# Kernel optimization log

Measured on AMD Instinct MI355X. Metric: run time of the kernel, lower is better.

Reference implementation:

```python
import jax, jax.numpy as jnp
from jax import lax
import numpy as np

B, T, C_IN, H, W = 2, 4, 128, 64, 64
D_MODEL, N_Q, N_POINTS, PATCH, N_LAYERS = 256, 300, 8, 3, 6


def _sine_pos(Hh, Ww, d, temperature=10000.0):
    # mask is all-False, so cumsum of ones -> arange(1..H)/H * 2pi
    two_pi = 2.0 * np.pi
    yn = (jnp.arange(1, Hh + 1, dtype=jnp.float32) / (Hh + 1e-6)) * two_pi
    xn = (jnp.arange(1, Ww + 1, dtype=jnp.float32) / (Ww + 1e-6)) * two_pi
    q = d // 4
    i = jnp.arange(q, dtype=jnp.float32)
    dim_t = temperature ** (2.0 * jnp.floor(i / 2.0) / q)
    py = yn[:, None] / dim_t
    px = xn[:, None] / dim_t
    py = jnp.stack([jnp.sin(py), jnp.cos(py)], axis=-1).reshape(Hh, 2 * q)
    px = jnp.stack([jnp.sin(px), jnp.cos(px)], axis=-1).reshape(Ww, 2 * q)
    pos = jnp.concatenate([
        jnp.broadcast_to(py[:, None, :], (Hh, Ww, 2 * q)),
        jnp.broadcast_to(px[None, :, :], (Hh, Ww, 2 * q)),
    ], axis=-1)
    return jnp.transpose(pos, (2, 0, 1))  # [d,H,W]


def _sample_scale(fmap, ref, ps):
    # fmap [B,C,h,w]; ref [B,nQ,nP,2] in [0,1]. Bilinear grid_sample,
    # padding_mode='border', align_corners=True -> direct gather (no replication).
    Bc, C, h, w = fmap.shape
    half = (ps - 1) / 2.0
    off = jnp.linspace(-half, half, ps, dtype=jnp.float32)
    oy, ox = jnp.meshgrid(off, off, indexing='ij')  # [ps,ps]
    gx = ref[..., 0, None, None] * 2.0 - 1.0 + ox * (2.0 / w)  # [B,nQ,nP,ps,ps]
    gy = ref[..., 1, None, None] * 2.0 - 1.0 + oy * (2.0 / h)
    x = jnp.clip((gx + 1.0) * 0.5 * (w - 1), 0.0, w - 1.0)
    y = jnp.clip((gy + 1.0) * 0.5 * (h - 1), 0.0, h - 1.0)
    x0 = jnp.floor(x); y0 = jnp.floor(y)
    wx = x - x0; wy = y - y0
    x0i = x0.astype(jnp.int32); y0i = y0.astype(jnp.int32)
    x1i = jnp.minimum(x0i + 1, w - 1); y1i = jnp.minimum(y0i + 1, h - 1)

    def per_b(fb, y0b, x0b, y1b, x1b, wxb, wyb):
        v00 = fb[:, y0b, x0b]  # [C,nQ,nP,ps,ps]
        v01 = fb[:, y0b, x1b]
        v10 = fb[:, y1b, x0b]
        v11 = fb[:, y1b, x1b]
        return (v00 * (1 - wxb) * (1 - wyb) + v01 * wxb * (1 - wyb)
                + v10 * (1 - wxb) * wyb + v11 * wxb * wyb)

    out = jax.vmap(per_b)(fmap, y0i, x0i, y1i, x1i, wx, wy)  # [B,C,nQ,nP,ps,ps]
    return jnp.transpose(out, (0, 2, 3, 4, 5, 1))  # [B,nQ,nP,ps,ps,C]


def reference(feat, pred_boxes_init, w_tf, b_tf, w_in, b_in, w_lat, b_lat, w_sm, b_sm,
              q_embed, q_pos, Wq, bq, Wo, bo, Wp1, bp1, Wp2, bp2,
              w_r1, b_r1, w_r2, b_r2, w_b1, b_b1, w_b2, b_b2, w_cls, b_cls):
    Bb, Tt, Cin, Hh, Ww = feat.shape
    d = w_in.shape[0]
    nP = w_r2.shape[0] // 2
    ps = int(round((Wp1.shape[-1] // d) ** 0.5))
    # temporal fuse: Conv3d kernel (3,1,1), padding (1,0,0)
    x = lax.conv_general_dilated(jnp.transpose(feat, (0, 2, 1, 3, 4)), w_tf,
                                 (1, 1, 1), [(1, 1), (0, 0), (0, 0)],
                                 dimension_numbers=('NCDHW', 'OIDHW', 'NCDHW'))
    x = x + b_tf[None, :, None, None, None]
    x = x.mean(axis=2)  # [B,Cin,H,W]
    x = jnp.einsum('bchw,dc->bdhw', x, w_in) + b_in[None, :, None, None]
    x = x + _sine_pos(Hh, Ww, d)[None]
    # FPN over scales {1,2,4}: avg_pool -> 1x1 lateral -> 3x3 smooth
    feats = []
    for i, s in enumerate((1, 2, 4)):
        xi = x if s == 1 else x.reshape(Bb, d, Hh // s, s, Ww // s, s).mean(axis=(3, 5))
        xi = jnp.einsum('bchw,oc->bohw', xi, w_lat[i]) + b_lat[i][None, :, None, None]
        xi = lax.conv_general_dilated(xi, w_sm[i], (1, 1), [(1, 1), (1, 1)],
                                      dimension_numbers=('NCHW', 'OIHW', 'NCHW'))
        xi = xi + b_sm[i][None, :, None, None]
        feats.append(xi)
    nQ = q_embed.shape[0]
    queries = jnp.broadcast_to((q_embed + q_pos)[None], (Bb, nQ, d))
    boxes = pred_boxes_init
    inv_sqrt_d = 1.0 / float(np.sqrt(d))
    for l in range(Wq.shape[0]):
        h1 = jax.nn.relu(jnp.einsum('bqd,od->bqo', queries, w_r1) + b_r1)
        ro = jnp.tanh(jnp.einsum('bqd,od->bqo', h1, w_r2) + b_r2)
        ro = ro.reshape(Bb, nQ, nP, 2) * 0.5
        ref = jnp.clip(boxes[:, :, None, :2] + ro, 0.0, 1.0)
        sampled = jnp.concatenate([_sample_scale(f, ref, ps) for f in feats], axis=2)
        sampled = sampled[:, :, :nP]  # truncate multi-scale concat back to nP
        flat = sampled.reshape(Bb, nQ, nP, ps * ps * d)
        pv = jax.nn.relu(jnp.einsum('bqpi,oi->bqpo', flat, Wp1[l]) + bp1[l])
        pv = jnp.einsum('bqpd,od->bqpo', pv, Wp2[l]) + bp2[l]
        kv = pv.mean(axis=2)  # [B,nP_q,d] -> [B,nQ,d]
        q = jnp.einsum('bqd,od->bqo', queries, Wq[l]) + bq[l]
        attn = jax.nn.softmax(jnp.einsum('bqd,bkd->bqk', q, kv) * inv_sqrt_d, axis=-1)
        out = jnp.einsum('bqk,bkd->bqd', attn, kv)
        queries = queries + (jnp.einsum('bqd,od->bqo', out, Wo[l]) + bo[l])
        hb = jax.nn.relu(jnp.einsum('bqd,od->bqo', queries, w_b1) + b_b1)
        delta = jax.nn.sigmoid(jnp.einsum('bqd,od->bqo', hb, w_b2) + b_b2)
        boxes = jnp.clip(boxes + 0.1 * jnp.tanh(delta - 0.5), 0.0, 1.0)
    logits = (jnp.einsum('bqd,od->bqo', queries, w_cls) + b_cls)[..., 0]
    return logits, boxes


def setup_inputs() -> dict:
    key = jax.random.key(0)
    keys = iter(jax.random.split(key, 48))

    def nrm(shape, s=0.02):
        return jax.random.normal(next(keys), shape, dtype=jnp.float32) * s

    inp = {
        'feat': jax.random.normal(next(keys), (B, T, C_IN, H, W), dtype=jnp.float32),
        'pred_boxes_init': jax.random.uniform(next(keys), (B, N_Q, 4), dtype=jnp.float32),
        'w_tf': nrm((C_IN, C_IN, 3, 1, 1)), 'b_tf': jnp.zeros((C_IN,), jnp.float32),
        'w_in': nrm((D_MODEL, C_IN)), 'b_in': jnp.zeros((D_MODEL,), jnp.float32),
        'w_lat': nrm((3, D_MODEL, D_MODEL)), 'b_lat': jnp.zeros((3, D_MODEL), jnp.float32),
        'w_sm': nrm((3, D_MODEL, D_MODEL, 3, 3)), 'b_sm': jnp.zeros((3, D_MODEL), jnp.float32),
        'q_embed': nrm((N_Q, D_MODEL), 1.0), 'q_pos': nrm((N_Q, D_MODEL), 1.0),
        'Wq': nrm((N_LAYERS, D_MODEL, D_MODEL)), 'bq': jnp.zeros((N_LAYERS, D_MODEL), jnp.float32),
        'Wo': nrm((N_LAYERS, D_MODEL, D_MODEL)), 'bo': jnp.zeros((N_LAYERS, D_MODEL), jnp.float32),
        'Wp1': nrm((N_LAYERS, D_MODEL, PATCH * PATCH * D_MODEL)), 'bp1': jnp.zeros((N_LAYERS, D_MODEL), jnp.float32),
        'Wp2': nrm((N_LAYERS, D_MODEL, D_MODEL)), 'bp2': jnp.zeros((N_LAYERS, D_MODEL), jnp.float32),
        'w_r1': nrm((D_MODEL, D_MODEL)), 'b_r1': jnp.zeros((D_MODEL,), jnp.float32),
        'w_r2': nrm((2 * N_POINTS, D_MODEL)), 'b_r2': jnp.zeros((2 * N_POINTS,), jnp.float32),
        'w_b1': nrm((D_MODEL, D_MODEL)), 'b_b1': jnp.zeros((D_MODEL,), jnp.float32),
        'w_b2': nrm((4, D_MODEL)), 'b_b2': jnp.zeros((4,), jnp.float32),
        'w_cls': nrm((1, D_MODEL)), 'b_cls': jnp.zeros((1,), jnp.float32),
    }
    return inp
```

## Files before the change

### kernel.cpp

```cpp
#include <hip/hip_runtime.h>
#include <hip/hip_bf16.h>
#include <math.h>

#define BB 2
#define TT 4
#define CIN 128
#define DM 256
#define NQ 300
#define NP 8
#define PS 3
#define NL 6
#define HW 4096
#define KP 2304

typedef __attribute__((ext_vector_type(8))) short short8;
typedef __attribute__((ext_vector_type(4))) short short4_t;
typedef __attribute__((ext_vector_type(4))) float f32x4;
typedef unsigned short ushort_t;

static __device__ __forceinline__ ushort_t f2bf(float f) {
  __hip_bfloat16 h = __float2bfloat16(f);
  return *reinterpret_cast<ushort_t*>(&h);
}
static __device__ __forceinline__ float bf2f(ushort_t u) {
  return __uint_as_float(((unsigned)u) << 16);
}

__global__ void k_prep(const float* __restrict__ w_in, const float* __restrict__ w_lat,
                       const float* __restrict__ Wp2, const float* __restrict__ Wo,
                       const float* __restrict__ w_b1, const float* __restrict__ Wp1,
                       ushort_t* __restrict__ win_bf, ushort_t* __restrict__ wlat_bf,
                       ushort_t* __restrict__ wp2_bf, ushort_t* __restrict__ wo_bf,
                       ushort_t* __restrict__ wb1_bf, ushort_t* __restrict__ wp1_bf,
                       const float* __restrict__ w_tf, ushort_t* __restrict__ tct,
                       const float* __restrict__ w_sm, ushort_t* __restrict__ wsm_bf,
                       const float* __restrict__ w_r1, const float* __restrict__ Wq,
                       ushort_t* __restrict__ wqr_bf,
                       const float* __restrict__ b_r1, const float* __restrict__ bq,
                       float* __restrict__ bqr,
                       uint4* __restrict__ x2p_zero,
                       const float* __restrict__ b_tf, const float* __restrict__ b_in,
                       float* __restrict__ bias_comb,
                       const float* __restrict__ qe, const float* __restrict__ qp,
                       const float* __restrict__ pb, float* __restrict__ queries,
                       ushort_t* __restrict__ qbf, float* __restrict__ boxes) {
  __shared__ float bt[128];
  int b = blockIdx.x, t = threadIdx.x;
  if (b < 4385) {
    int i = b * 256 + t;
    const float* s; ushort_t* d; int base;
    if (i < 8192)         { s = w_in;  d = win_bf;  base = 0; }
    else if (i < 24576)   { s = w_lat; d = wlat_bf; base = 8192; }
    else if (i < 122880)  { s = Wp2;   d = wp2_bf;  base = 24576; }
    else if (i < 221184)  { s = Wo;    d = wo_bf;   base = 122880; }
    else if (i < 237568)  { s = w_b1;  d = wb1_bf;  base = 221184; }
    else if (i < 1122304) { s = Wp1;   d = wp1_bf;  base = 237568; }
    else return;
    int j = i - base;
    float4 v = ((const float4*)s)[j];
    d[j * 4 + 0] = f2bf(v.x);
    d[j * 4 + 1] = f2bf(v.y);
    d[j * 4 + 2] = f2bf(v.z);
    d[j * 4 + 3] = f2bf(v.w);
  } else if (b < 4641) {
    int i = (b - 4385) * 256 + t;
    int k = i >> 7, c = i & 127;
    int u = k >> 7, ci = k & 127;
    const float* wp = w_tf + ((size_t)(c * 128 + ci)) * 3;
    float w0 = wp[0], w1 = wp[1], w2 = wp[2];
    float coef = (u == 0) ? (w0 + w1) : (u == 3) ? (w1 + w2) : (w0 + w1 + w2);
    tct[(size_t)k * 128 + c] = f2bf(0.25f * coef);
  } else if (b < 6945) {
    int i = (b - 4641) * 256 + t;
    int n = i / KP;
    int r = i - n * KP;
    int tp = r >> 8, c = r & 255;
    wsm_bf[i] = f2bf(w_sm[((size_t)(n * 256 + c)) * 9 + tp]);
  } else if (b < 10017) {
    int i = (b - 6945) * 256 + t;
    int l = i / (512 * 256);
    int r = i - l * 512 * 256;
    int n = r >> 8, c = r & 255;
    float v = (n < 256) ? w_r1[n * 256 + c] : Wq[((size_t)l * 256 + (n - 256)) * 256 + c];
    wqr_bf[i] = f2bf(v);
  } else if (b < 10029) {
    int i = (b - 10017) * 256 + t;
    if (i >= NL * 512) return;
    int l = i >> 9, n = i & 511;
    bqr[i] = (n < 256) ? b_r1[n] : bq[l * 256 + n - 256];
  } else if (b < 11118) {
    int j = (b - 10029) * 256 + t;
    if (j < 278784) x2p_zero[j] = make_uint4(0u, 0u, 0u, 0u);
  } else if (b < 11119) {
    int d = t;
    if (d < 128) bt[d] = b_tf[d];
    __syncthreads();
    float a = b_in[d];
    for (int c = 0; c < 128; ++c) a += w_in[d * 128 + c] * bt[c];
    bias_comb[d] = a;
  } else {
    int i = (b - 11119) * 256 + t;
    if (i < BB * NQ * DM) {
      int rd = i % (NQ * DM);
      float v = qe[rd] + qp[rd];
      queries[i] = v;
      qbf[i] = f2bf(v);
    }
    if (i < BB * NQ * 4) boxes[i] = pb[i];
  }
}

__global__ __launch_bounds__(256) void k_tr(const float* __restrict__ feat,
                                            ushort_t* __restrict__ featT) {
  __shared__ float ldsF[64][65];
  int tid = threadIdx.x;
  int gs = blockIdx.x;
  int b = gs >> 6;
  int s0 = (gs & 63) * 64;
  int k0 = blockIdx.y * 64;
  int kk = tid >> 2, sc0 = (tid & 3) * 16;
  {
    int k = k0 + kk;
    int u = k >> 7, ci = k & 127;
    const float* src = feat + (((size_t)(b * 4 + u) * 128 + ci) << 12) + s0 + sc0;
#pragma unroll
    for (int j = 0; j < 4; ++j) {
      float4 v = *(const float4*)(src + j * 4);
      ldsF[kk][sc0 + j * 4 + 0] = v.x;
      ldsF[kk][sc0 + j * 4 + 1] = v.y;
      ldsF[kk][sc0 + j * 4 + 2] = v.z;
      ldsF[kk][sc0 + j * 4 + 3] = v.w;
    }
  }
  __syncthreads();
#pragma unroll
  for (int p = 0; p < 2; ++p) {
    int idx = p * 256 + tid;
    int s_l = idx >> 3, kc = (idx & 7) * 8;
    short8 v;
#pragma unroll
    for (int j = 0; j < 8; ++j) v[j] = (short)f2bf(ldsF[kc + j][s_l]);
    *(short8*)(featT + (size_t)(b * 4096 + s0 + s_l) * 512 + k0 + kc) = v;
  }
}

__global__ __launch_bounds__(256) void k_feat2(const ushort_t* __restrict__ featT,
                                               const ushort_t* __restrict__ wcomb,
                                               const float* __restrict__ biasc,
                                               ushort_t* __restrict__ xcl) {
  __shared__ ushort_t As[32 * 36];
  __shared__ ushort_t Bs[64 * 36];
  __shared__ float dimt_s[256];
  int tid = threadIdx.x;
  {
    int dd = tid & 127;
    int ii = dd >> 1;
    dimt_s[tid] = powf(10000.0f, (2.0f * (float)(ii >> 1)) / 64.0f);
  }
  int bm = blockIdx.x * 32, bn = blockIdx.y * 64;
  int w = tid >> 6, lane = tid & 63;
  int wm = (w & 1) * 16, wn = (w >> 1) * 32;
  int q = lane >> 4, ml = lane & 15;
  int sra = tid >> 3, sca = (tid & 7) * 4;
  int srb = tid >> 2, scb = (tid & 3) * 8;
  const ushort_t* Ag = featT + (size_t)(bm + sra) * 512 + sca;
  const ushort_t* Wg = wcomb + (size_t)(bn + srb) * 512 + scb;
  f32x4 acc[2] = {};
  short4_t av = *(const short4_t*)Ag;
  short8 wv = *(const short8*)Wg;
  for (int k0 = 0; k0 < 512; k0 += 32) {
    *(short4_t*)(As + sra * 36 + sca) = av;
    *(short8*)(Bs + srb * 36 + scb) = wv;
    __syncthreads();
    if (k0 + 32 < 512) {
      av = *(const short4_t*)(Ag + k0 + 32);
      wv = *(const short8*)(Wg + k0 + 32);
    }
    short8 a = *(const short8*)(As + (wm + ml) * 36 + q * 8);
    short8 b0 = *(const short8*)(Bs + (wn + ml) * 36 + q * 8);
    short8 b1 = *(const short8*)(Bs + (wn + 16 + ml) * 36 + q * 8);
    acc[0] = __builtin_amdgcn_mfma_f32_16x16x32_bf16(a, b0, acc[0], 0, 0, 0);
    acc[1] = __builtin_amdgcn_mfma_f32_16x16x32_bf16(a, b1, acc[1], 0, 0, 0);
    __syncthreads();
  }
  const float FKT = 6.28318530717958647692f / 64.000001f;
#pragma unroll
  for (int j = 0; j < 2; ++j) {
    int cn = bn + wn + j * 16 + ml;
    float dimt = dimt_s[cn];
    float bC = biasc[cn];
    bool isx = cn >= 128;
    bool isc = cn & 1;
#pragma unroll
    for (int r = 0; r < 4; ++r) {
      int rm = bm + wm + q * 4 + r;
      int s = rm & 4095;
      int y = s >> 6, x = s & 63;
      float ang = (float)((isx ? x : y) + 1) * FKT / dimt;
      float pos = isc ? cosf(ang) : sinf(ang);
      xcl[(size_t)rm * 256 + cn] = f2bf(acc[j][r] + bC + pos);
    }
  }
}

template <int ACT, int OUTMODE, int MG>
__global__ __launch_bounds__(256) void k_gemm_bf16(const ushort_t* __restrict__ A,
                                                   const ushort_t* __restrict__ W,
                                                   const float* __restrict__ bias,
                                                   const float* __restrict__ res,
                                                   float* __restrict__ Cf,
                                                   ushort_t* __restrict__ Cb,
                                                   int M, int N, int K,
                                                   const ushort_t* __restrict__ W2,
                                                   const float* __restrict__ bias2) {
  __shared__ ushort_t As[64 * 36];
  __shared__ ushort_t Bs[64 * 36];
  int tid = threadIdx.x;
  int bm = blockIdx.x * 64, bn = blockIdx.y * 64;
  int w = tid >> 6, lane = tid & 63;
  int wm = (w & 1) * 32, wn = (w >> 1) * 32;
  int q = lane >> 4, ml = lane & 15;
  f32x4 acc[2][2] = {};
  int srow = tid >> 2, scol = (tid & 3) * 8;
  int ga = bm + srow;
  if (MG) ga = min(ga, M - 1);
  const ushort_t* Ag = A + (size_t)ga * K + scol;
  const ushort_t* Wg;
  if (OUTMODE == 7 && bn >= 256) Wg = W2 + (size_t)(bn - 256 + srow) * K + scol;
  else Wg = W + (size_t)(bn + srow) * K + scol;
  for (int k0 = 0; k0 < K; k0 += 32) {
    short8 av = *(const short8*)(Ag + k0);
    short8 wv = *(const short8*)(Wg + k0);
    *(short8*)(As + srow * 36 + scol) = av;
    *(short8*)(Bs + srow * 36 + scol) = wv;
    __syncthreads();
    short8 a0 = *(const short8*)(As + (wm + ml) * 36 + q * 8);
    short8 a1 = *(const short8*)(As + (wm + 16 + ml) * 36 + q * 8);
    short8 b0 = *(const short8*)(Bs + (wn + ml) * 36 + q * 8);
    short8 b1 = *(const short8*)(Bs + (wn + 16 + ml) * 36 + q * 8);
    acc[0][0] = __builtin_amdgcn_mfma_f32_16x16x32_bf16(a0, b0, acc[0][0], 0, 0, 0);
    acc[0][1] = __builtin_amdgcn_mfma_f32_16x16x32_bf16(a0, b1, acc[0][1], 0, 0, 0);
    acc[1][0] = __builtin_amdgcn_mfma_f32_16x16x32_bf16(a1, b0, acc[1][0], 0, 0, 0);
    acc[1][1] = __builtin_amdgcn_mfma_f32_16x16x32_bf16(a1, b1, acc[1][1], 0, 0, 0);
    __syncthreads();
  }
#pragma unroll
  for (int i = 0; i < 2; ++i) {
#pragma unroll
    for (int j = 0; j < 2; ++j) {
      int cn = bn + wn + j * 16 + ml;
      float bsv;
      if (OUTMODE == 7) bsv = (cn < 256) ? bias[cn] : bias2[cn - 256];
      else bsv = bias ? bias[cn] : 0.f;
#pragma unroll
      for (int r = 0; r < 4; ++r) {
        int rm = bm + wm + i * 16 + q * 4 + r;
        if (MG && rm >= M) continue;
        float v = acc[i][j][r] + bsv;
        if (OUTMODE == 0) {
          if (ACT == 1) v = fmaxf(v, 0.f);
          Cf[(size_t)rm * N + cn] = v;
        } else if (OUTMODE == 1) {
          int b = rm >> 12, rem = rm & 4095;
          int y = rem >> 6, xx = rem & 63;
          Cb[(((size_t)(b * 66 + y + 1)) * 66 + xx + 1) * 256 + cn] = f2bf(v);
        } else if (OUTMODE == 2) {
          v += res[(size_t)rm * N + cn];
          Cf[(size_t)rm * N + cn] = v;
          Cb[(size_t)rm * N + cn] = f2bf(v);
        } else if (OUTMODE == 4) {
          if (cn < 256) Cf[(size_t)rm * 256 + cn] = fmaxf(v, 0.f);
          else Cb[(size_t)rm * 256 + cn - 256] = f2bf(v);
        } else if (OUTMODE == 6) {
          Cb[(size_t)rm * N + cn] = f2bf(v);
        } else if (OUTMODE == 7) {
          if (cn < 256) Cf[(size_t)rm * 256 + cn] = fmaxf(v, 0.f);
          else if (cn < 512) ((float*)Cb)[(size_t)rm * 256 + cn - 256] = fmaxf(v, 0.f);
          else ((ushort_t*)res)[(size_t)rm * 256 + cn - 512] = f2bf(v);
        }
      }
    }
  }
}

__global__ __launch_bounds__(256) void k_wp1_split(const ushort_t* __restrict__ A,
                                                   const ushort_t* __restrict__ W,
                                                   float* __restrict__ part) {
  __shared__ ushort_t As[64 * 36];
  __shared__ ushort_t Bs[64 * 36];
  int tid = threadIdx.x;
  int bm = blockIdx.x * 64, bn = blockIdx.y * 64;
  int kz = blockIdx.z * 768;
  int w = tid >> 6, lane = tid & 63;
  int wm = (w & 1) * 32, wn = (w >> 1) * 32;
  int q = lane >> 4, ml = lane & 15;
  int srow = tid >> 2, scol = (tid & 3) * 8;
  const ushort_t* Ag = A + (size_t)(bm + srow) * KP + kz + scol;
  const ushort_t* Wg = W + (size_t)(bn + srow) * KP + kz + scol;
  f32x4 acc[2][2] = {};
  short8 av = *(const short8*)(Ag);
  short8 wv = *(const short8*)(Wg);
  for (int k0 = 0; k0 < 768; k0 += 32) {
    *(short8*)(As + srow * 36 + scol) = av;
    *(short8*)(Bs + srow * 36 + scol) = wv;
    __syncthreads();
    if (k0 + 32 < 768) {
      av = *(const short8*)(Ag + k0 + 32);
      wv = *(const short8*)(Wg + k0 + 32);
    }
    short8 a0 = *(const short8*)(As + (wm + ml) * 36 + q * 8);
    short8 a1 = *(const short8*)(As + (wm + 16 + ml) * 36 + q * 8);
    short8 b0 = *(const short8*)(Bs + (wn + ml) * 36 + q * 8);
    short8 b1 = *(const short8*)(Bs + (wn + 16 + ml) * 36 + q * 8);
    acc[0][0] = __builtin_amdgcn_mfma_f32_16x16x32_bf16(a0, b0, acc[0][0], 0, 0, 0);
    acc[0][1] = __builtin_amdgcn_mfma_f32_16x16x32_bf16(a0, b1, acc[0][1], 0, 0, 0);
    acc[1][0] = __builtin_amdgcn_mfma_f32_16x16x32_bf16(a1, b0, acc[1][0], 0, 0, 0);
    acc[1][1] = __builtin_amdgcn_mfma_f32_16x16x32_bf16(a1, b1, acc[1][1], 0, 0, 0);
    __syncthreads();
  }
  float* pz = part + (size_t)blockIdx.z * 4800 * 256;
#pragma unroll
  for (int i = 0; i < 2; ++i)
#pragma unroll
    for (int j = 0; j < 2; ++j) {
      int cn = bn + wn + j * 16 + ml;
#pragma unroll
      for (int r = 0; r < 4; ++r) {
        int rm = bm + wm + i * 16 + q * 4 + r;
        pz[(size_t)rm * 256 + cn] = acc[i][j][r];
      }
    }
}

__global__ __launch_bounds__(256) void k_wp1_reduce(const float* __restrict__ part,
                                                    const float* __restrict__ bias,
                                                    ushort_t* __restrict__ pvm) {
  int row = blockIdx.x;
  int d = threadIdx.x;
  float b = bias[d];
  float s = 0.f;
#pragma unroll
  for (int p = 0; p < 8; ++p) {
    size_t idx = (size_t)(row * 8 + p) * 256 + d;
    float v = part[idx] + part[idx + (size_t)4800 * 256] +
              part[idx + (size_t)2 * 4800 * 256] + b;
    s += fmaxf(v, 0.f);
  }
  pvm[(size_t)row * 256 + d] = f2bf(s * 0.125f);
}

__global__ __launch_bounds__(256) void k_conv3(const ushort_t* __restrict__ x2p,
                                               const ushort_t* __restrict__ wsm,
                                               const float* __restrict__ bsm,
                                               ushort_t* __restrict__ fcl) {
  __shared__ ushort_t As[32 * 36];
  __shared__ ushort_t Bs[64 * 36];
  int tid = threadIdx.x;
  int bm = blockIdx.x * 32, bn = blockIdx.y * 64;
  int w = tid >> 6, lane = tid & 63;
  int wm = (w & 1) * 16, wn = (w >> 1) * 32;
  int q = lane >> 4, ml = lane & 15;
  int sra = tid >> 3, sca = (tid & 7) * 4;
  int srb = tid >> 2, scb = (tid & 3) * 8;
  int sA = bm + sra;
  int b = sA >> 12, rem = sA & 4095;
  size_t pbase = ((size_t)(b * 66 + (rem >> 6)) * 66 + (rem & 63)) * 256;
  const ushort_t* Wg = wsm + (size_t)(bn + srb) * KP + scb;
  auto loadA = [&](int k0) {
    int ka = k0 + sca;
    int t9 = ka >> 8;
    int ky = t9 / 3, kx = t9 - ky * 3;
    return *(const short4_t*)(x2p + pbase + (size_t)(ky * 66 + kx) * 256 + (ka & 255));
  };
  f32x4 acc[2] = {};
  short4_t av = loadA(0);
  short8 wv = *(const short8*)(Wg);
  for (int k0 = 0; k0 < KP; k0 += 32) {
    *(short4_t*)(As + sra * 36 + sca) = av;
    *(short8*)(Bs + srb * 36 + scb) = wv;
    __syncthreads();
    if (k0 + 32 < KP) {
      av = loadA(k0 + 32);
      wv = *(const short8*)(Wg + k0 + 32);
    }
    short8 a = *(const short8*)(As + (wm + ml) * 36 + q * 8);
    short8 b0 = *(const short8*)(Bs + (wn + ml) * 36 + q * 8);
    short8 b1 = *(const short8*)(Bs + (wn + 16 + ml) * 36 + q * 8);
    acc[0] = __builtin_amdgcn_mfma_f32_16x16x32_bf16(a, b0, acc[0], 0, 0, 0);
    acc[1] = __builtin_amdgcn_mfma_f32_16x16x32_bf16(a, b1, acc[1], 0, 0, 0);
    __syncthreads();
  }
#pragma unroll
  for (int j = 0; j < 2; ++j) {
    int cn = bn + wn + j * 16 + ml;
    float bsv = bsm[cn];
#pragma unroll
    for (int r = 0; r < 4; ++r) {
      int rm = bm + wm + q * 4 + r;
      fcl[(size_t)rm * 256 + cn] = f2bf(acc[j][r] + bsv);
    }
  }
}

__global__ __launch_bounds__(256) void k_sample(const ushort_t* __restrict__ fcl,
                                                const float* __restrict__ h1,
                                                const float* __restrict__ w_r2,
                                                const float* __restrict__ b_r2,
                                                const float* __restrict__ boxes,
                                                ushort_t* __restrict__ flat) {
  __shared__ float pr[8];
  __shared__ float bc2[2];
  int blk = blockIdx.x;
  int row = blk >> 3, p = blk & 7;
  int b = row / NQ;
  int tid = threadIdx.x;
  float h = h1[(size_t)row * 256 + tid];
  float px = h * w_r2[(size_t)(2 * p) * 256 + tid];
  float py = h * w_r2[(size_t)(2 * p + 1) * 256 + tid];
#pragma unroll
  for (int s = 32; s > 0; s >>= 1) {
    px += __shfl_down(px, s, 64);
    py += __shfl_down(py, s, 64);
  }
  int w = tid >> 6, lane = tid & 63;
  if (lane == 0) { pr[w * 2] = px; pr[w * 2 + 1] = py; }
  __syncthreads();
  if (tid == 0) {
    float sx = pr[0] + pr[2] + pr[4] + pr[6] + b_r2[2 * p];
    float sy = pr[1] + pr[3] + pr[5] + pr[7] + b_r2[2 * p + 1];
    float rx = boxes[row * 4 + 0] + 0.5f * tanhf(sx);
    float ry = boxes[row * 4 + 1] + 0.5f * tanhf(sy);
    bc2[0] = fminf(fmaxf(rx, 0.f), 1.f);
    bc2[1] = fminf(fmaxf(ry, 0.f), 1.f);
  }
  __syncthreads();
  float rx = bc2[0], ry = bc2[1];
  int c = tid;
  const ushort_t* fb = fcl + (size_t)b * HW * DM;
  ushort_t* op = flat + (size_t)blk * KP;
#pragma unroll
  for (int jy = 0; jy < 3; ++jy) {
    float yy = (ry + (float)(jy - 1) * (1.0f / 64.0f)) * 63.0f;
    yy = fminf(fmaxf(yy, 0.f), 63.0f);
    float y0f = floorf(yy);
    float wy = yy - y0f;
    int y0 = (int)y0f;
    int y1 = min(y0 + 1, 63);
#pragma unroll
    for (int jx = 0; jx < 3; ++jx) {
      float xx = (rx + (float)(jx - 1) * (1.0f / 64.0f)) * 63.0f;
      xx = fminf(fmaxf(xx, 0.f), 63.0f);
      float x0f = floorf(xx);
      float wx = xx - x0f;
      int x0 = (int)x0f;
      int x1 = min(x0 + 1, 63);
      float v00 = bf2f(fb[(y0 * 64 + x0) * DM + c]);
      float v01 = bf2f(fb[(y0 * 64 + x1) * DM + c]);
      float v10 = bf2f(fb[(y1 * 64 + x0) * DM + c]);
      float v11 = bf2f(fb[(y1 * 64 + x1) * DM + c]);
      float v = v00 * (1.f - wx) * (1.f - wy) + v01 * wx * (1.f - wy) +
                v10 * (1.f - wx) * wy + v11 * wx * wy;
      op[(jy * 3 + jx) * DM + c] = f2bf(v);
    }
  }
}

__global__ __launch_bounds__(256) void k_attn(const ushort_t* __restrict__ qb2,
                                              const ushort_t* __restrict__ kvb,
                                              ushort_t* __restrict__ ao) {
  __shared__ float qs[256];
  __shared__ float sc[512];
  __shared__ float red[256];
  int row = blockIdx.x;
  int b = row / NQ;
  int tid = threadIdx.x;
  qs[tid] = bf2f(qb2[(size_t)row * DM + tid]);
  __syncthreads();
  const ushort_t* kvB = kvb + (size_t)b * NQ * DM;
#pragma unroll
  for (int s2 = 0; s2 < 2; ++s2) {
    int k = tid + s2 * 256;
    float v = -1e30f;
    if (k < NQ) {
      const ushort_t* kp = kvB + (size_t)k * DM;
      float a = 0.f;
#pragma unroll
      for (int d = 0; d < 256; d += 8) {
        short8 k8 = *(const short8*)(kp + d);
        const float* qd = qs + d;
        a += bf2f((ushort_t)k8[0]) * qd[0];
        a += bf2f((ushort_t)k8[1]) * qd[1];
        a += bf2f((ushort_t)k8[2]) * qd[2];
        a += bf2f((ushort_t)k8[3]) * qd[3];
        a += bf2f((ushort_t)k8[4]) * qd[4];
        a += bf2f((ushort_t)k8[5]) * qd[5];
        a += bf2f((ushort_t)k8[6]) * qd[6];
        a += bf2f((ushort_t)k8[7]) * qd[7];
      }
      v = a * (1.0f / 16.0f);
    }
    sc[k] = v;
  }
  __syncthreads();
  red[tid] = fmaxf(sc[tid], sc[tid + 256]);
  __syncthreads();
  for (int st = 128; st > 0; st >>= 1) {
    if (tid < st) red[tid] = fmaxf(red[tid], red[tid + st]);
    __syncthreads();
  }
  float mx = red[0];
  __syncthreads();
  float e0 = (tid < NQ) ? expf(sc[tid] - mx) : 0.f;
  float e1 = (tid + 256 < NQ) ? expf(sc[tid + 256] - mx) : 0.f;
  sc[tid] = e0;
  sc[tid + 256] = e1;
  red[tid] = e0 + e1;
  __syncthreads();
  for (int st = 128; st > 0; st >>= 1) {
    if (tid < st) red[tid] += red[tid + st];
    __syncthreads();
  }
  float inv = 1.0f / red[0];
  __syncthreads();
  float acc = 0.f;
#pragma unroll 4
  for (int k = 0; k < NQ; ++k)
    acc += sc[k] * bf2f(kvB[(size_t)k * DM + tid]);
  ao[(size_t)row * DM + tid] = f2bf(acc * inv);
}

__global__ __launch_bounds__(256) void k_boxf(const float* __restrict__ hb,
                                              const float* __restrict__ w_b2,
                                              const float* __restrict__ b_b2,
                                              float* __restrict__ boxes,
                                              int last,
                                              const float* __restrict__ queries,
                                              const float* __restrict__ w_cls,
                                              const float* __restrict__ b_cls,
                                              float* __restrict__ out) {
  __shared__ float nb[4];
  int row = blockIdx.x;
  int tid = threadIdx.x;
  int j = tid >> 6, lane = tid & 63;
  float4 hv = *(const float4*)(hb + (size_t)row * 256 + lane * 4);
  float4 wv = *(const float4*)(w_b2 + (size_t)j * 256 + lane * 4);
  float aa = hv.x * wv.x + hv.y * wv.y + hv.z * wv.z + hv.w * wv.w;
#pragma unroll
  for (int s = 32; s > 0; s >>= 1) aa += __shfl_down(aa, s, 64);
  if (lane == 0) {
    aa += b_b2[j];
    float delta = 1.0f / (1.0f + expf(-aa));
    float v = boxes[row * 4 + j] + 0.1f * tanhf(delta - 0.5f);
    v = fminf(fmaxf(v, 0.f), 1.f);
    boxes[row * 4 + j] = v;
    nb[j] = v;
  }
  if (last) {
    __syncthreads();
    if (j == 0) {
      float4 qv = *(const float4*)(queries + (size_t)row * 256 + lane * 4);
      float4 cv = *(const float4*)(w_cls + lane * 4);
      float a2 = qv.x * cv.x + qv.y * cv.y + qv.z * cv.z + qv.w * cv.w;
#pragma unroll
      for (int s = 32; s > 0; s >>= 1) a2 += __shfl_down(a2, s, 64);
      if (lane == 0) out[row] = a2 + b_cls[0];
    } else if (j == 1 && lane < 4) {
      out[600 + row * 4 + lane] = nb[lane];
    }
  }
}

extern "C" void kernel_launch(void* const* d_in, const int* in_sizes, int n_in,
                              void* d_out, int out_size, void* d_ws, size_t ws_size,
                              hipStream_t stream) {
  const float* feat   = (const float*)d_in[0];
  const float* pb     = (const float*)d_in[1];
  const float* w_tf   = (const float*)d_in[2];
  const float* b_tf   = (const float*)d_in[3];
  const float* w_in   = (const float*)d_in[4];
  const float* b_in   = (const float*)d_in[5];
  const float* w_lat  = (const float*)d_in[6];
  const float* b_lat  = (const float*)d_in[7];
  const float* w_sm   = (const float*)d_in[8];
  const float* b_sm   = (const float*)d_in[9];
  const float* q_embed= (const float*)d_in[10];
  const float* q_pos  = (const float*)d_in[11];
  const float* Wq     = (const float*)d_in[12];
  const float* bq     = (const float*)d_in[13];
  const float* Wo     = (const float*)d_in[14];
  const float* bo     = (const float*)d_in[15];
  const float* Wp1    = (const float*)d_in[16];
  const float* bp1    = (const float*)d_in[17];
  const float* Wp2    = (const float*)d_in[18];
  const float* bp2    = (const float*)d_in[19];
  const float* w_r1   = (const float*)d_in[20];
  const float* b_r1   = (const float*)d_in[21];
  const float* w_r2   = (const float*)d_in[22];
  const float* b_r2   = (const float*)d_in[23];
  const float* w_b1   = (const float*)d_in[24];
  const float* b_b1   = (const float*)d_in[25];
  const float* w_b2   = (const float*)d_in[26];
  const float* b_b2   = (const float*)d_in[27];
  const float* w_cls  = (const float*)d_in[28];
  const float* b_cls  = (const float*)d_in[29];
  float* out = (float*)d_out;

  float* ws = (float*)d_ws;
  size_t off = 0;
  auto alloc = [&](size_t n) { float* p = ws + off; off += n; return p; };
  ushort_t* flat    = (ushort_t*)alloc(5529600);
  float*    part    = alloc(3686400);
  ushort_t* featT   = (ushort_t*)alloc(2097152);
  ushort_t* xcl     = (ushort_t*)alloc(1048576);
  ushort_t* x2p     = (ushort_t*)alloc(1115136);
  ushort_t* fcl     = (ushort_t*)alloc(1048576);
  ushort_t* wcomb   = (ushort_t*)alloc(65536);
  ushort_t* tct     = (ushort_t*)alloc(32768);
  ushort_t* win_bf  = (ushort_t*)alloc(16384);
  float*    biasc   = alloc(256);
  ushort_t* wlat_bf = (ushort_t*)alloc(32768);
  ushort_t* wsm_bf  = (ushort_t*)alloc(294912);
  ushort_t* wp1_bf  = (ushort_t*)alloc(1769472);
  ushort_t* wqr_bf  = (ushort_t*)alloc(393216);
  float*    bqr     = alloc(3072);
  ushort_t* wp2_bf  = (ushort_t*)alloc(196608);
  ushort_t* wo_bf   = (ushort_t*)alloc(196608);
  ushort_t* wb1_bf  = (ushort_t*)alloc(32768);
  float* queries = alloc(153600);
  ushort_t* qbf  = (ushort_t*)alloc(76800);
  float* h1      = alloc(153600);
  ushort_t* qb2  = (ushort_t*)alloc(76800);
  ushort_t* kvb  = (ushort_t*)alloc(76800);
  ushort_t* ao   = (ushort_t*)alloc(76800);
  float* hb      = alloc(153600);
  ushort_t* pvm  = (ushort_t*)alloc(76800);
  float* boxes   = alloc(2400);
  (void)ws_size; (void)in_sizes; (void)n_in; (void)out_size;

  k_prep<<<11719, 256, 0, stream>>>(w_in, w_lat, Wp2, Wo, w_b1, Wp1,
                                    win_bf, wlat_bf, wp2_bf, wo_bf, wb1_bf, wp1_bf,
                                    w_tf, tct, w_sm, wsm_bf, w_r1, Wq, wqr_bf,
                                    b_r1, bq, bqr,
                                    (uint4*)x2p, b_tf, b_in, biasc,
                                    q_embed, q_pos, pb, queries, qbf, boxes);
  k_gemm_bf16<0, 6, 0><<<dim3(4, 8), 256, 0, stream>>>(win_bf, tct, nullptr, nullptr,
                                                       nullptr, wcomb, 256, 512, 128,
                                                       nullptr, nullptr);
  k_tr<<<dim3(128, 8), 256, 0, stream>>>(feat, featT);
  k_feat2<<<dim3(256, 4), 256, 0, stream>>>(featT, wcomb, biasc, xcl);
  k_gemm_bf16<0, 1, 0><<<dim3(128, 4), 256, 0, stream>>>(xcl, wlat_bf, b_lat, nullptr,
                                                         nullptr, x2p, BB * HW, 256, 256,
                                                         nullptr, nullptr);
  k_conv3<<<dim3(256, 4), 256, 0, stream>>>(x2p, wsm_bf, b_sm, fcl);

  const int M6 = BB * NQ;
  const int Mp = BB * NQ * NP;
  dim3 g600((M6 + 63) / 64, 4);
  dim3 g600w((M6 + 63) / 64, 8);
  dim3 g600m((M6 + 63) / 64, 12);
  dim3 gsk(Mp / 64, 4, 3);

  k_gemm_bf16<0, 4, 1><<<g600w, 256, 0, stream>>>(qbf, wqr_bf, bqr, nullptr, h1,
                                                  qb2, M6, 512, 256,
                                                  nullptr, nullptr);
  for (int l = 0; l < NL; ++l) {
    k_sample<<<Mp, 256, 0, stream>>>(fcl, h1, w_r2, b_r2, boxes, flat);
    k_wp1_split<<<gsk, 256, 0, stream>>>(flat, wp1_bf + (size_t)l * 256 * KP, part);
    k_wp1_reduce<<<600, 256, 0, stream>>>(part, bp1 + (size_t)l * DM, pvm);
    k_gemm_bf16<0, 6, 1><<<g600, 256, 0, stream>>>(pvm, wp2_bf + (size_t)l * DM * DM,
                                                   bp2 + (size_t)l * DM, nullptr, nullptr,
                                                   kvb, M6, DM, DM, nullptr, nullptr);
    k_attn<<<M6, 256, 0, stream>>>(qb2, kvb, ao);
    k_gemm_bf16<0, 2, 1><<<g600, 256, 0, stream>>>(ao, wo_bf + (size_t)l * DM * DM,
                                                   bo + (size_t)l * DM, queries, queries,
                                                   qbf, M6, DM, DM, nullptr, nullptr);
    int ln = (l + 1) % NL;
    k_gemm_bf16<0, 7, 1><<<g600m, 256, 0, stream>>>(qbf, wb1_bf, b_b1, (const float*)qb2,
                                                    hb, (ushort_t*)h1, M6, 768, 256,
                                                    wqr_bf + (size_t)ln * 512 * 256,
                                                    bqr + ln * 512);
    k_boxf<<<M6, 256, 0, stream>>>(hb, w_b2, b_b2, boxes, (l == NL - 1) ? 1 : 0,
                                   queries, w_cls, b_cls, out);
  }
}
```

Measured before the change: 775.2 us.

## Fold Wp2 into query and output projections, store split-K partials in bf16

Removes the per-layer Wp2 GEMM by algebraically composing it into the attention path. The query projection is pre-multiplied by Wp2, so scores use pvm directly. Wo is composed with Wp2 into a fused output weight, with matching fused biases computed in a new compose kernel at setup. Split-K partials for Wp1 are also stored as bf16 to halve that traffic, at the cost of extra rounding from bf16-composed weights and partials.

```diff
diff --git a/kernel.cpp b/kernel.cpp
--- a/kernel.cpp
+++ b/kernel.cpp
@@ -27,17 +27,18 @@
 }
 
 __global__ void k_prep(const float* __restrict__ w_in, const float* __restrict__ w_lat,
-                       const float* __restrict__ Wp2, const float* __restrict__ Wo,
-                       const float* __restrict__ w_b1, const float* __restrict__ Wp1,
+                       const float* __restrict__ Wo, const float* __restrict__ w_b1,
+                       const float* __restrict__ w_r1, const float* __restrict__ Wp1,
                        ushort_t* __restrict__ win_bf, ushort_t* __restrict__ wlat_bf,
-                       ushort_t* __restrict__ wp2_bf, ushort_t* __restrict__ wo_bf,
-                       ushort_t* __restrict__ wb1_bf, ushort_t* __restrict__ wp1_bf,
+                       ushort_t* __restrict__ wo_bf, ushort_t* __restrict__ wb1_bf,
+                       ushort_t* __restrict__ wr1_bf, ushort_t* __restrict__ wp1_bf,
                        const float* __restrict__ w_tf, ushort_t* __restrict__ tct,
                        const float* __restrict__ w_sm, ushort_t* __restrict__ wsm_bf,
-                       const float* __restrict__ w_r1, const float* __restrict__ Wq,
-                       ushort_t* __restrict__ wqr_bf,
-                       const float* __restrict__ b_r1, const float* __restrict__ bq,
-                       float* __restrict__ bqr,
+                       const float* __restrict__ Wp2, const float* __restrict__ Wq,
+                       ushort_t* __restrict__ wp2t, ushort_t* __restrict__ wqT,
+                       const float* __restrict__ bq, const float* __restrict__ bp2,
+                       const float* __restrict__ bo,
+                       float* __restrict__ bqt, float* __restrict__ bfuse,
                        uint4* __restrict__ x2p_zero,
                        const float* __restrict__ b_tf, const float* __restrict__ b_in,
                        float* __restrict__ bias_comb,
@@ -46,52 +47,67 @@
                        ushort_t* __restrict__ qbf, float* __restrict__ boxes) {
   __shared__ float bt[128];
   int b = blockIdx.x, t = threadIdx.x;
-  if (b < 4385) {
+  if (b < 4064) {
     int i = b * 256 + t;
     const float* s; ushort_t* d; int base;
     if (i < 8192)         { s = w_in;  d = win_bf;  base = 0; }
     else if (i < 24576)   { s = w_lat; d = wlat_bf; base = 8192; }
-    else if (i < 122880)  { s = Wp2;   d = wp2_bf;  base = 24576; }
-    else if (i < 221184)  { s = Wo;    d = wo_bf;   base = 122880; }
-    else if (i < 237568)  { s = w_b1;  d = wb1_bf;  base = 221184; }
-    else if (i < 1122304) { s = Wp1;   d = wp1_bf;  base = 237568; }
-    else return;
+    else if (i < 122880)  { s = Wo;    d = wo_bf;   base = 24576; }
+    else if (i < 139264)  { s = w_b1;  d = wb1_bf;  base = 122880; }
+    else if (i < 155648)  { s = w_r1;  d = wr1_bf;  base = 139264; }
+    else                  { s = Wp1;   d = wp1_bf;  base = 155648; }
     int j = i - base;
     float4 v = ((const float4*)s)[j];
     d[j * 4 + 0] = f2bf(v.x);
     d[j * 4 + 1] = f2bf(v.y);
     d[j * 4 + 2] = f2bf(v.z);
     d[j * 4 + 3] = f2bf(v.w);
-  } else if (b < 4641) {
-    int i = (b - 4385) * 256 + t;
+  } else if (b < 4320) {
+    int i = (b - 4064) * 256 + t;
     int k = i >> 7, c = i & 127;
     int u = k >> 7, ci = k & 127;
     const float* wp = w_tf + ((size_t)(c * 128 + ci)) * 3;
     float w0 = wp[0], w1 = wp[1], w2 = wp[2];
     float coef = (u == 0) ? (w0 + w1) : (u == 3) ? (w1 + w2) : (w0 + w1 + w2);
     tct[(size_t)k * 128 + c] = f2bf(0.25f * coef);
-  } else if (b < 6945) {
-    int i = (b - 4641) * 256 + t;
+  } else if (b < 6624) {
+    int i = (b - 4320) * 256 + t;
     int n = i / KP;
     int r = i - n * KP;
     int tp = r >> 8, c = r & 255;
     wsm_bf[i] = f2bf(w_sm[((size_t)(n * 256 + c)) * 9 + tp]);
-  } else if (b < 10017) {
-    int i = (b - 6945) * 256 + t;
-    int l = i / (512 * 256);
-    int r = i - l * 512 * 256;
-    int n = r >> 8, c = r & 255;
-    float v = (n < 256) ? w_r1[n * 256 + c] : Wq[((size_t)l * 256 + (n - 256)) * 256 + c];
-    wqr_bf[i] = f2bf(v);
-  } else if (b < 10029) {
-    int i = (b - 10017) * 256 + t;
-    if (i >= NL * 512) return;
-    int l = i >> 9, n = i & 511;
-    bqr[i] = (n < 256) ? b_r1[n] : bq[l * 256 + n - 256];
-  } else if (b < 11118) {
-    int j = (b - 10029) * 256 + t;
+  } else if (b < 9696) {
+    int i = (b - 6624) * 256 + t;
+    if (i < 393216) {
+      int l = i >> 16, r = i & 65535;
+      int d = r >> 8, o = r & 255;
+      wp2t[i] = f2bf(Wp2[((size_t)(l * 256 + o)) * 256 + d]);
+    } else {
+      int j = i - 393216;
+      int l = j >> 16, r = j & 65535;
+      int c = r >> 8, o = r & 255;
+      wqT[j] = f2bf(Wq[((size_t)(l * 256 + o)) * 256 + c]);
+    }
+  } else if (b < 9708) {
+    int i = (b - 9696) * 256 + t;
+    if (i < 1536) {
+      int l = i >> 8, d = i & 255;
+      float a = 0.f;
+      for (int o = 0; o < 256; ++o)
+        a += bq[l * 256 + o] * Wp2[((size_t)(l * 256 + o)) * 256 + d];
+      bqt[i] = a;
+    } else {
+      int j = i - 1536;
+      int l = j >> 8, o2 = j & 255;
+      float a = bo[l * 256 + o2];
+      for (int o = 0; o < 256; ++o)
+        a += bp2[l * 256 + o] * Wo[((size_t)(l * 256 + o2)) * 256 + o];
+      bfuse[j] = a;
+    }
+  } else if (b < 10797) {
+    int j = (b - 9708) * 256 + t;
     if (j < 278784) x2p_zero[j] = make_uint4(0u, 0u, 0u, 0u);
-  } else if (b < 11119) {
+  } else if (b < 10798) {
     int d = t;
     if (d < 128) bt[d] = b_tf[d];
     __syncthreads();
@@ -99,7 +115,7 @@
     for (int c = 0; c < 128; ++c) a += w_in[d * 128 + c] * bt[c];
     bias_comb[d] = a;
   } else {
-    int i = (b - 11119) * 256 + t;
+    int i = (b - 10798) * 256 + t;
     if (i < BB * NQ * DM) {
       int rd = i % (NQ * DM);
       float v = qe[rd] + qp[rd];
@@ -108,6 +124,57 @@
     }
     if (i < BB * NQ * 4) boxes[i] = pb[i];
   }
+}
+
+__global__ __launch_bounds__(256) void k_wcompose(const ushort_t* __restrict__ wp2t,
+                                                  const ushort_t* __restrict__ wqT,
+                                                  const ushort_t* __restrict__ wo_bf,
+                                                  ushort_t* __restrict__ wqt,
+                                                  ushort_t* __restrict__ wfuse) {
+  __shared__ ushort_t As[64 * 36];
+  __shared__ ushort_t Bs[64 * 36];
+  int z = blockIdx.z, l = z % 6;
+  const ushort_t* A;
+  const ushort_t* W;
+  ushort_t* C;
+  if (z < 6) { A = wp2t + l * 65536; W = wqT + l * 65536; C = wqt + l * 65536; }
+  else       { A = wo_bf + l * 65536; W = wp2t + l * 65536; C = wfuse + l * 65536; }
+  int tid = threadIdx.x;
+  int bm = blockIdx.x * 64, bn = blockIdx.y * 64;
+  int w = tid >> 6, lane = tid & 63;
+  int wm = (w & 1) * 32, wn = (w >> 1) * 32;
+  int q = lane >> 4, ml = lane & 15;
+  f32x4 acc[2][2] = {};
+  int srow = tid >> 2, scol = (tid & 3) * 8;
+  const ushort_t* Ag = A + (size_t)(bm + srow) * 256 + scol;
+  const ushort_t* Wg = W + (size_t)(bn + srow) * 256 + scol;
+  for (int k0 = 0; k0 < 256; k0 += 32) {
+    short8 av = *(const short8*)(Ag + k0);
+    short8 wv = *(const short8*)(Wg + k0);
+    *(short8*)(As + srow * 36 + scol) = av;
+    *(short8*)(Bs + srow * 36 + scol) = wv;
+    __syncthreads();
+    short8 a0 = *(const short8*)(As + (wm + ml) * 36 + q * 8);
+    short8 a1 = *(const short8*)(As + (wm + 16 + ml) * 36 + q * 8);
+    short8 b0 = *(const short8*)(Bs + (wn + ml) * 36 + q * 8);
+    short8 b1 = *(const short8*)(Bs + (wn + 16 + ml) * 36 + q * 8);
+    acc[0][0] = __builtin_amdgcn_mfma_f32_16x16x32_bf16(a0, b0, acc[0][0], 0, 0, 0);
+    acc[0][1] = __builtin_amdgcn_mfma_f32_16x16x32_bf16(a0, b1, acc[0][1], 0, 0, 0);
+    acc[1][0] = __builtin_amdgcn_mfma_f32_16x16x32_bf16(a1, b0, acc[1][0], 0, 0, 0);
+    acc[1][1] = __builtin_amdgcn_mfma_f32_16x16x32_bf16(a1, b1, acc[1][1], 0, 0, 0);
+    __syncthreads();
+  }
+#pragma unroll
+  for (int i = 0; i < 2; ++i)
+#pragma unroll
+    for (int j = 0; j < 2; ++j) {
+      int cn = bn + wn + j * 16 + ml;
+#pragma unroll
+      for (int r = 0; r < 4; ++r) {
+        int rm = bm + wm + i * 16 + q * 4 + r;
+        C[(size_t)rm * 256 + cn] = f2bf(acc[i][j][r]);
+      }
+    }
 }
 
 __global__ __launch_bounds__(256) void k_tr(const float* __restrict__ feat,
@@ -212,7 +279,9 @@
                                                    ushort_t* __restrict__ Cb,
                                                    int M, int N, int K,
                                                    const ushort_t* __restrict__ W2,
-                                                   const float* __restrict__ bias2) {
+                                                   const float* __restrict__ bias2,
+                                                   const ushort_t* __restrict__ W3,
+                                                   const float* __restrict__ bias3) {
   __shared__ ushort_t As[64 * 36];
   __shared__ ushort_t Bs[64 * 36];
   int tid = threadIdx.x;
@@ -226,8 +295,16 @@
   if (MG) ga = min(ga, M - 1);
   const ushort_t* Ag = A + (size_t)ga * K + scol;
   const ushort_t* Wg;
-  if (OUTMODE == 7 && bn >= 256) Wg = W2 + (size_t)(bn - 256 + srow) * K + scol;
-  else Wg = W + (size_t)(bn + srow) * K + scol;
+  if (OUTMODE == 7) {
+    int seg = bn >> 8;
+    const ushort_t* Wb = (seg == 0) ? W : ((seg == 1) ? W2 : W3);
+    Wg = Wb + (size_t)((bn & 255) + srow) * K + scol;
+  } else if (OUTMODE == 4) {
+    const ushort_t* Wb = (bn < 256) ? W : W2;
+    Wg = Wb + (size_t)((bn & 255) + srow) * K + scol;
+  } else {
+    Wg = W + (size_t)(bn + srow) * K + scol;
+  }
   for (int k0 = 0; k0 < K; k0 += 32) {
     short8 av = *(const short8*)(Ag + k0);
     short8 wv = *(const short8*)(Wg + k0);
@@ -250,8 +327,14 @@
     for (int j = 0; j < 2; ++j) {
       int cn = bn + wn + j * 16 + ml;
       float bsv;
-      if (OUTMODE == 7) bsv = (cn < 256) ? bias[cn] : bias2[cn - 256];
-      else bsv = bias ? bias[cn] : 0.f;
+      if (OUTMODE == 7) {
+        int seg = cn >> 8;
+        bsv = ((seg == 0) ? bias : ((seg == 1) ? bias2 : bias3))[cn & 255];
+      } else if (OUTMODE == 4) {
+        bsv = ((cn < 256) ? bias : bias2)[cn & 255];
+      } else {
+        bsv = bias ? bias[cn] : 0.f;
+      }
 #pragma unroll
       for (int r = 0; r < 4; ++r) {
         int rm = bm + wm + i * 16 + q * 4 + r;
@@ -270,13 +353,13 @@
           Cb[(size_t)rm * N + cn] = f2bf(v);
         } else if (OUTMODE == 4) {
           if (cn < 256) Cf[(size_t)rm * 256 + cn] = fmaxf(v, 0.f);
-          else Cb[(size_t)rm * 256 + cn - 256] = f2bf(v);
+          else Cb[(size_t)rm * 256 + (cn & 255)] = f2bf(v);
         } else if (OUTMODE == 6) {
           Cb[(size_t)rm * N + cn] = f2bf(v);
         } else if (OUTMODE == 7) {
           if (cn < 256) Cf[(size_t)rm * 256 + cn] = fmaxf(v, 0.f);
-          else if (cn < 512) ((float*)Cb)[(size_t)rm * 256 + cn - 256] = fmaxf(v, 0.f);
-          else ((ushort_t*)res)[(size_t)rm * 256 + cn - 512] = f2bf(v);
+          else if (cn < 512) ((float*)Cb)[(size_t)rm * 256 + (cn & 255)] = fmaxf(v, 0.f);
+          else ((ushort_t*)res)[(size_t)rm * 256 + (cn & 255)] = f2bf(v);
         }
       }
     }
@@ -285,7 +368,7 @@
 
 __global__ __launch_bounds__(256) void k_wp1_split(const ushort_t* __restrict__ A,
                                                    const ushort_t* __restrict__ W,
-                                                   float* __restrict__ part) {
+                                                   ushort_t* __restrict__ part) {
   __shared__ ushort_t As[64 * 36];
   __shared__ ushort_t Bs[64 * 36];
   int tid = threadIdx.x;
@@ -318,7 +401,7 @@
     acc[1][1] = __builtin_amdgcn_mfma_f32_16x16x32_bf16(a1, b1, acc[1][1], 0, 0, 0);
     __syncthreads();
   }
-  float* pz = part + (size_t)blockIdx.z * 4800 * 256;
+  ushort_t* pz = part + (size_t)blockIdx.z * 4800 * 256;
 #pragma unroll
   for (int i = 0; i < 2; ++i)
 #pragma unroll
@@ -327,12 +410,12 @@
 #pragma unroll
       for (int r = 0; r < 4; ++r) {
         int rm = bm + wm + i * 16 + q * 4 + r;
-        pz[(size_t)rm * 256 + cn] = acc[i][j][r];
+        pz[(size_t)rm * 256 + cn] = f2bf(acc[i][j][r]);
       }
     }
 }
 
-__global__ __launch_bounds__(256) void k_wp1_reduce(const float* __restrict__ part,
+__global__ __launch_bounds__(256) void k_wp1_reduce(const ushort_t* __restrict__ part,
                                                     const float* __restrict__ bias,
                                                     ushort_t* __restrict__ pvm) {
   int row = blockIdx.x;
@@ -342,8 +425,8 @@
 #pragma unroll
   for (int p = 0; p < 8; ++p) {
     size_t idx = (size_t)(row * 8 + p) * 256 + d;
-    float v = part[idx] + part[idx + (size_t)4800 * 256] +
-              part[idx + (size_t)2 * 4800 * 256] + b;
+    float v = bf2f(part[idx]) + bf2f(part[idx + (size_t)4800 * 256]) +
+              bf2f(part[idx + (size_t)2 * 4800 * 256]) + b;
     s += fmaxf(v, 0.f);
   }
   pvm[(size_t)row * 256 + d] = f2bf(s * 0.125f);
@@ -465,18 +548,18 @@
   }
 }
 
-__global__ __launch_bounds__(256) void k_attn(const ushort_t* __restrict__ qb2,
-                                              const ushort_t* __restrict__ kvb,
-                                              ushort_t* __restrict__ ao) {
+__global__ __launch_bounds__(256) void k_attn(const ushort_t* __restrict__ qt,
+                                              const ushort_t* __restrict__ pvm,
+                                              ushort_t* __restrict__ ctx) {
   __shared__ float qs[256];
   __shared__ float sc[512];
   __shared__ float red[256];
   int row = blockIdx.x;
   int b = row / NQ;
   int tid = threadIdx.x;
-  qs[tid] = bf2f(qb2[(size_t)row * DM + tid]);
-  __syncthreads();
-  const ushort_t* kvB = kvb + (size_t)b * NQ * DM;
+  qs[tid] = bf2f(qt[(size_t)row * DM + tid]);
+  __syncthreads();
+  const ushort_t* kvB = pvm + (size_t)b * NQ * DM;
 #pragma unroll
   for (int s2 = 0; s2 < 2; ++s2) {
     int k = tid + s2 * 256;
@@ -526,7 +609,7 @@
 #pragma unroll 4
   for (int k = 0; k < NQ; ++k)
     acc += sc[k] * bf2f(kvB[(size_t)k * DM + tid]);
-  ao[(size_t)row * DM + tid] = f2bf(acc * inv);
+  ctx[(size_t)row * DM + tid] = f2bf(acc * inv);
 }
 
 __global__ __launch_bounds__(256) void k_boxf(const float* __restrict__ hb,
@@ -609,7 +692,7 @@
   size_t off = 0;
   auto alloc = [&](size_t n) { float* p = ws + off; off += n; return p; };
   ushort_t* flat    = (ushort_t*)alloc(5529600);
-  float*    part    = alloc(3686400);
+  ushort_t* part    = (ushort_t*)alloc(1843200);
   ushort_t* featT   = (ushort_t*)alloc(2097152);
   ushort_t* xcl     = (ushort_t*)alloc(1048576);
   ushort_t* x2p     = (ushort_t*)alloc(1115136);
@@ -621,36 +704,42 @@
   ushort_t* wlat_bf = (ushort_t*)alloc(32768);
   ushort_t* wsm_bf  = (ushort_t*)alloc(294912);
   ushort_t* wp1_bf  = (ushort_t*)alloc(1769472);
-  ushort_t* wqr_bf  = (ushort_t*)alloc(393216);
-  float*    bqr     = alloc(3072);
-  ushort_t* wp2_bf  = (ushort_t*)alloc(196608);
   ushort_t* wo_bf   = (ushort_t*)alloc(196608);
   ushort_t* wb1_bf  = (ushort_t*)alloc(32768);
+  ushort_t* wr1_bf  = (ushort_t*)alloc(32768);
+  ushort_t* wp2t    = (ushort_t*)alloc(196608);
+  ushort_t* wqT     = (ushort_t*)alloc(196608);
+  ushort_t* wqt_bf  = (ushort_t*)alloc(196608);
+  ushort_t* wfuse_bf= (ushort_t*)alloc(196608);
+  float*    bqt     = alloc(1536);
+  float*    bfuse   = alloc(1536);
   float* queries = alloc(153600);
   ushort_t* qbf  = (ushort_t*)alloc(76800);
   float* h1      = alloc(153600);
-  ushort_t* qb2  = (ushort_t*)alloc(76800);
-  ushort_t* kvb  = (ushort_t*)alloc(76800);
-  ushort_t* ao   = (ushort_t*)alloc(76800);
+  ushort_t* qt   = (ushort_t*)alloc(76800);
+  ushort_t* ctx  = (ushort_t*)alloc(76800);
   float* hb      = alloc(153600);
   ushort_t* pvm  = (ushort_t*)alloc(76800);
   float* boxes   = alloc(2400);
   (void)ws_size; (void)in_sizes; (void)n_in; (void)out_size;
 
-  k_prep<<<11719, 256, 0, stream>>>(w_in, w_lat, Wp2, Wo, w_b1, Wp1,
-                                    win_bf, wlat_bf, wp2_bf, wo_bf, wb1_bf, wp1_bf,
-                                    w_tf, tct, w_sm, wsm_bf, w_r1, Wq, wqr_bf,
-                                    b_r1, bq, bqr,
+  k_prep<<<11398, 256, 0, stream>>>(w_in, w_lat, Wo, w_b1, w_r1, Wp1,
+                                    win_bf, wlat_bf, wo_bf, wb1_bf, wr1_bf, wp1_bf,
+                                    w_tf, tct, w_sm, wsm_bf,
+                                    Wp2, Wq, wp2t, wqT,
+                                    bq, bp2, bo, bqt, bfuse,
                                     (uint4*)x2p, b_tf, b_in, biasc,
                                     q_embed, q_pos, pb, queries, qbf, boxes);
   k_gemm_bf16<0, 6, 0><<<dim3(4, 8), 256, 0, stream>>>(win_bf, tct, nullptr, nullptr,
                                                        nullptr, wcomb, 256, 512, 128,
-                                                       nullptr, nullptr);
+                                                       nullptr, nullptr, nullptr, nullptr);
+  k_wcompose<<<dim3(4, 4, 12), 256, 0, stream>>>(wp2t, wqT, wo_bf, wqt_bf, wfuse_bf);
+
   k_tr<<<dim3(128, 8), 256, 0, stream>>>(feat, featT);
   k_feat2<<<dim3(256, 4), 256, 0, stream>>>(featT, wcomb, biasc, xcl);
   k_gemm_bf16<0, 1, 0><<<dim3(128, 4), 256, 0, stream>>>(xcl, wlat_bf, b_lat, nullptr,
                                                          nullptr, x2p, BB * HW, 256, 256,
-                                                         nullptr, nullptr);
+                                                         nullptr, nullptr, nullptr, nullptr);
   k_conv3<<<dim3(256, 4), 256, 0, stream>>>(x2p, wsm_bf, b_sm, fcl);
 
   const int M6 = BB * NQ;
@@ -660,25 +749,24 @@
   dim3 g600m((M6 + 63) / 64, 12);
   dim3 gsk(Mp / 64, 4, 3);
 
-  k_gemm_bf16<0, 4, 1><<<g600w, 256, 0, stream>>>(qbf, wqr_bf, bqr, nullptr, h1,
-                                                  qb2, M6, 512, 256,
-                                                  nullptr, nullptr);
+  k_gemm_bf16<0, 4, 1><<<g600w, 256, 0, stream>>>(qbf, wr1_bf, b_r1, nullptr, h1,
+                                                  qt, M6, 512, 256,
+                                                  wqt_bf, bqt, nullptr, nullptr);
   for (int l = 0; l < NL; ++l) {
     k_sample<<<Mp, 256, 0, stream>>>(fcl, h1, w_r2, b_r2, boxes, flat);
     k_wp1_split<<<gsk, 256, 0, stream>>>(flat, wp1_bf + (size_t)l * 256 * KP, part);
     k_wp1_reduce<<<600, 256, 0, stream>>>(part, bp1 + (size_t)l * DM, pvm);
-    k_gemm_bf16<0, 6, 1><<<g600, 256, 0, stream>>>(pvm, wp2_bf + (size_t)l * DM * DM,
-                                                   bp2 + (size_t)l * DM, nullptr, nullptr,
-                                                   kvb, M6, DM, DM, nullptr, nullptr);
-    k_attn<<<M6, 256, 0, stream>>>(qb2, kvb, ao);
-    k_gemm_bf16<0, 2, 1><<<g600, 256, 0, stream>>>(ao, wo_bf + (size_t)l * DM * DM,
-                                                   bo + (size_t)l * DM, queries, queries,
-                                                   qbf, M6, DM, DM, nullptr, nullptr);
+    k_attn<<<M6, 256, 0, stream>>>(qt, pvm, ctx);
+    k_gemm_bf16<0, 2, 1><<<g600, 256, 0, stream>>>(ctx, wfuse_bf + (size_t)l * 65536,
+                                                   bfuse + l * 256, queries, queries,
+                                                   qbf, M6, DM, DM,
+                                                   nullptr, nullptr, nullptr, nullptr);
     int ln = (l + 1) % NL;
-    k_gemm_bf16<0, 7, 1><<<g600m, 256, 0, stream>>>(qbf, wb1_bf, b_b1, (const float*)qb2,
+    k_gemm_bf16<0, 7, 1><<<g600m, 256, 0, stream>>>(qbf, wb1_bf, b_b1, (const float*)qt,
                                                     hb, (ushort_t*)h1, M6, 768, 256,
-                                                    wqr_bf + (size_t)ln * 512 * 256,
-                                                    bqr + ln * 512);
+                                                    wr1_bf, b_r1,
+                                                    wqt_bf + (size_t)ln * 65536,
+                                                    bqt + ln * 256);
     k_boxf<<<M6, 256, 0, stream>>>(hb, w_b2, b_b2, boxes, (l == NL - 1) ? 1 : 0,
                                    queries, w_cls, b_cls, out);
   }
```

New measurement: 730.0 us. 1.06x faster.
